# Kernel optimization log

Measured on AMD Instinct MI355X. Metric: run time of the kernel, lower is better.

The kernel has to match this reference:

```python
import jax, jax.numpy as jnp
import numpy as np

N_NODES = 100000
N_EDGES = 1600000
IN_DIM, HID, OUT_DIM = 512, 32, 40


def setup_inputs() -> dict:
    key = jax.random.key(0)
    ks = jax.random.split(key, 6)
    x = jax.random.normal(ks[0], (N_NODES, IN_DIM), dtype=jnp.float32)
    edge_index = jax.random.randint(ks[1], (2, N_EDGES), 0, N_NODES, dtype=jnp.int64)
    # Glorot-ish init for the linear weights
    W1 = jax.random.normal(ks[2], (IN_DIM, HID), dtype=jnp.float32) / np.sqrt(IN_DIM)
    b1 = jnp.zeros((HID,), dtype=jnp.float32)
    W2 = jax.random.normal(ks[3], (HID, OUT_DIM), dtype=jnp.float32) / np.sqrt(HID)
    b2 = jnp.zeros((OUT_DIM,), dtype=jnp.float32)
    return {"x": x, "edge_index": edge_index, "W1": W1, "b1": b1, "W2": W2, "b2": b2}


def gcn_conv(x, W, b, src, dst, n_nodes):
    """PyG GCNConv: h = D^{-1/2} (A + I) D^{-1/2} (x W) + b."""
    h = x @ W  # linear transform first (reduces edge-level traffic)
    # add self-loops
    loop = jnp.arange(n_nodes, dtype=src.dtype)
    s = jnp.concatenate([src, loop])
    d = jnp.concatenate([dst, loop])
    # symmetric normalization from in-degree (including self-loops)
    deg = jax.ops.segment_sum(jnp.ones_like(d, dtype=h.dtype), d, num_segments=n_nodes)
    dinv = jnp.where(deg > 0, jax.lax.rsqrt(deg), 0.0)
    norm = dinv[s] * dinv[d]  # [E+N]
    msg = h[s] * norm[:, None]  # gather + scale
    out = jax.ops.segment_sum(msg, d, num_segments=n_nodes)  # scatter-add
    return out + b


def reference(x, edge_index, W1, b1, W2, b2):
    src, dst = edge_index[0], edge_index[1]
    n = x.shape[0]
    h = jax.nn.relu(gcn_conv(x, W1, b1, src, dst, n))
    # dropout is identity in eval mode (reference runs in eval)
    out = gcn_conv(h, W2, b2, src, dst, n)
    return out
```

## Files before the change

kernel.cpp:

```cpp
#include <hip/hip_runtime.h>
#include <hip/hip_bf16.h>

#define N_IN 512
#define HID 32
#define OUTD 40
#define NCOPY 8

typedef __attribute__((ext_vector_type(8))) short bf16x8;
typedef __attribute__((ext_vector_type(4))) float f32x4;
typedef __attribute__((ext_vector_type(8))) _Float16 half8;


__global__ void k_init(int* __restrict__ csr, int tot4, int* __restrict__ cnt8,
                       int n8_4, int n, _Float16* __restrict__ g1, _Float16* __restrict__ p)
{
    int i = blockIdx.x * blockDim.x + threadIdx.x;
    if (i < tot4) {
        int4 v = make_int4(n, n, n, n);
        *(int4*)&csr[(size_t)i * 4] = v;
    }
    if (i < n8_4) {
        int4 z4 = make_int4(0, 0, 0, 0);
        *(int4*)&cnt8[(size_t)i * 4] = z4;
    }
    if (blockIdx.x == 0) {
        float4 z = make_float4(0.f, 0.f, 0.f, 0.f);
        if (threadIdx.x < 4)
            ((float4*)&g1[(size_t)n * HID])[threadIdx.x] = z;
        else if (threadIdx.x < 8)
            ((float4*)&p[(size_t)n * HID])[threadIdx.x - 4] = z;
    }
}

__global__ void k_count(const int* __restrict__ dst, int* __restrict__ cnt8,
                        int* __restrict__ rankp, int n, int e)
{
    int c = blockIdx.x & (NCOPY - 1);
    int* mycnt = cnt8 + (size_t)c * n;
    int i = (blockIdx.x * blockDim.x + threadIdx.x) * 4;
    if (i + 3 < e) {
        int4 d4 = *(const int4*)&dst[i];
        int r0 = atomicAdd(&mycnt[d4.x], 1);
        int r1 = atomicAdd(&mycnt[d4.y], 1);
        int r2 = atomicAdd(&mycnt[d4.z], 1);
        int r3 = atomicAdd(&mycnt[d4.w], 1);
        int hc = c << 24;
        *(int4*)&rankp[i] = make_int4(hc | r0, hc | r1, hc | r2, hc | r3);
    } else if (i < e) {
        for (int k = i; k < e; k++) {
            int r = atomicAdd(&mycnt[dst[k]], 1);
            rankp[k] = (c << 24) | r;
        }
    }
}

__global__ void k_bases(int* __restrict__ cnt8, int* __restrict__ cnt, int n)
{
    int d = blockIdx.x * blockDim.x + threadIdx.x;
    if (d >= n) return;
    int s = 0;
#pragma unroll
    for (int c = 0; c < NCOPY; c++) {
        int v = cnt8[(size_t)c * n + d];
        cnt8[(size_t)c * n + d] = s;
        s += v;
    }
    cnt[d] = s;
}

__global__ __launch_bounds__(256) void k_scan1(const int* __restrict__ cnt,
                                               int* __restrict__ offs,
                                               int* __restrict__ bsums, int n)
{
    __shared__ int sm[256];
    int t = threadIdx.x;
    int base = blockIdx.x * 1024 + t * 4;
    int a0 = (base + 0 < n) ? cnt[base + 0] : 0;
    int a1 = (base + 1 < n) ? cnt[base + 1] : 0;
    int a2 = (base + 2 < n) ? cnt[base + 2] : 0;
    int a3 = (base + 3 < n) ? cnt[base + 3] : 0;
    int d0 = (a0 + 15) & ~15;
    int d1 = (a1 + 15) & ~15;
    int d2 = (a2 + 15) & ~15;
    int d3 = (a3 + 15) & ~15;
    int s = d0 + d1 + d2 + d3;
    sm[t] = s;
    __syncthreads();
#pragma unroll
    for (int off = 1; off < 256; off <<= 1) {
        int v = (t >= off) ? sm[t - off] : 0;
        __syncthreads();
        sm[t] += v;
        __syncthreads();
    }
    int excl = sm[t] - s;
    if (base + 0 < n) offs[base + 0] = excl;
    if (base + 1 < n) offs[base + 1] = excl + d0;
    if (base + 2 < n) offs[base + 2] = excl + d0 + d1;
    if (base + 3 < n) offs[base + 3] = excl + d0 + d1 + d2;
    if (t == 255) bsums[blockIdx.x] = sm[255];
}

__global__ __launch_bounds__(256) void k_scan2(int* bsums, int nb)
{
    __shared__ int sm[256];
    int t = threadIdx.x;
    int s = (t < nb) ? bsums[t] : 0;
    sm[t] = s;
    __syncthreads();
#pragma unroll
    for (int off = 1; off < 256; off <<= 1) {
        int v = (t >= off) ? sm[t - off] : 0;
        __syncthreads();
        sm[t] += v;
        __syncthreads();
    }
    if (t < nb) bsums[t] = sm[t] - s;
}

__global__ void k_scan3(int* __restrict__ offs, const int* __restrict__ bsums,
                        const int* __restrict__ cnt, float* __restrict__ dinv, int n)
{
    int i = blockIdx.x * blockDim.x + threadIdx.x;
    if (i >= n) return;
    offs[i] = offs[i] + bsums[i >> 10];
    dinv[i] = rsqrtf((float)(cnt[i] + 1));
}

__global__ void k_posfill(const int* __restrict__ dst, const int* __restrict__ src,
                          const int* __restrict__ offs, const int* __restrict__ cnt8,
                          const int* __restrict__ rankp, int* __restrict__ csr,
                          int n, int e)
{
    int i = (blockIdx.x * blockDim.x + threadIdx.x) * 4;
    if (i >= e) return;
    if (i + 3 < e) {
        int4 d4 = *(const int4*)&dst[i];
        int4 rp = *(const int4*)&rankp[i];
        int4 s4 = *(const int4*)&src[i];
        int dd[4] = {d4.x, d4.y, d4.z, d4.w};
        int rr[4] = {rp.x, rp.y, rp.z, rp.w};
        int ss[4] = {s4.x, s4.y, s4.z, s4.w};
#pragma unroll
        for (int k = 0; k < 4; k++) {
            int d = dd[k];
            int c = ((unsigned)rr[k]) >> 24;
            int r = rr[k] & 0xFFFFFF;
            csr[offs[d] + cnt8[(size_t)c * n + d] + r] = ss[k];
        }
    } else {
        for (int k = i; k < e; k++) {
            int d = dst[k];
            int rv = rankp[k];
            int c = ((unsigned)rv) >> 24;
            int r = rv & 0xFFFFFF;
            csr[offs[d] + cnt8[(size_t)c * n + d] + r] = src[k];
        }
    }
}

__global__ void k_convw(const float* __restrict__ W, unsigned short* __restrict__ wfh,
                        unsigned short* __restrict__ wfl)
{
    int idx = blockIdx.x * blockDim.x + threadIdx.x;
    int j     = idx & 7;
    int lane  = (idx >> 3) & 63;
    int ntile = (idx >> 9) & 1;
    int kstep = idx >> 10;
    int k    = kstep * 32 + (lane >> 4) * 8 + j;
    int ncol = ntile * 16 + (lane & 15);
    float v = W[k * HID + ncol];
    unsigned u = __builtin_bit_cast(unsigned, v);
    unsigned short h = (unsigned short)(u >> 16);
    float hv = __builtin_bit_cast(float, u & 0xFFFF0000u);
    float rem = v - hv;
    unsigned ur = __builtin_bit_cast(unsigned, rem);
    ur += 0x7FFF + ((ur >> 16) & 1);
    wfh[idx] = h;
    wfl[idx] = (unsigned short)(ur >> 16);
}

__global__ __launch_bounds__(256) void k_gemm1(
    const float* __restrict__ x,
    const unsigned short* __restrict__ wfh, const unsigned short* __restrict__ wfl,
    const float* __restrict__ dinv, _Float16* __restrict__ g1, int n)
{
    const int t    = threadIdx.x;
    const int lane = t & 63;
    const int wave = t >> 6;
    const int m    = lane & 15;
    const int quad = lane >> 4;
    const int row0 = blockIdx.x * 64 + wave * 16;

    int arow = row0 + m;
    if (arow >= n) arow = n - 1;
    const float* xp = x + (size_t)arow * N_IN + quad * 8;

    f32x4 acc0 = {0.f, 0.f, 0.f, 0.f};
    f32x4 acc1 = {0.f, 0.f, 0.f, 0.f};

    for (int ks = 0; ks < 16; ks++) {
        float4 xa = *(const float4*)(xp + ks * 32);
        float4 xb = *(const float4*)(xp + ks * 32 + 4);
        float xe[8] = {xa.x, xa.y, xa.z, xa.w, xb.x, xb.y, xb.z, xb.w};
        bf16x8 ah, al;
#pragma unroll
        for (int j = 0; j < 8; j++) {
            unsigned u = __builtin_bit_cast(unsigned, xe[j]);
            ah[j] = (short)(u >> 16);
            float hv = __builtin_bit_cast(float, u & 0xFFFF0000u);
            float rem = xe[j] - hv;
            unsigned ur = __builtin_bit_cast(unsigned, rem);
            ur += 0x7FFF + ((ur >> 16) & 1);
            al[j] = (short)(ur >> 16);
        }
        bf16x8 bh0 = *(const bf16x8*)(wfh + ((size_t)(ks * 2 + 0) * 64 + lane) * 8);
        bf16x8 bh1 = *(const bf16x8*)(wfh + ((size_t)(ks * 2 + 1) * 64 + lane) * 8);
        bf16x8 bl0 = *(const bf16x8*)(wfl + ((size_t)(ks * 2 + 0) * 64 + lane) * 8);
        bf16x8 bl1 = *(const bf16x8*)(wfl + ((size_t)(ks * 2 + 1) * 64 + lane) * 8);

        acc0 = __builtin_amdgcn_mfma_f32_16x16x32_bf16(ah, bh0, acc0, 0, 0, 0);
        acc0 = __builtin_amdgcn_mfma_f32_16x16x32_bf16(al, bh0, acc0, 0, 0, 0);
        acc0 = __builtin_amdgcn_mfma_f32_16x16x32_bf16(ah, bl0, acc0, 0, 0, 0);
        acc1 = __builtin_amdgcn_mfma_f32_16x16x32_bf16(ah, bh1, acc1, 0, 0, 0);
        acc1 = __builtin_amdgcn_mfma_f32_16x16x32_bf16(al, bh1, acc1, 0, 0, 0);
        acc1 = __builtin_amdgcn_mfma_f32_16x16x32_bf16(ah, bl1, acc1, 0, 0, 0);
    }

#pragma unroll
    for (int r = 0; r < 4; r++) {
        int row = row0 + quad * 4 + r;
        if (row < n) {
            float dv = dinv[row];
            g1[(size_t)row * HID + m]      = (_Float16)(acc0[r] * dv);
            g1[(size_t)row * HID + 16 + m] = (_Float16)(acc1[r] * dv);
        }
    }
}


__global__ void k_agg1(const int* __restrict__ csr, const int* __restrict__ offs,
                       const int* __restrict__ cnt, const _Float16* __restrict__ g,
                       const float* __restrict__ dinv, const float* __restrict__ b1,
                       _Float16* __restrict__ p, int n)
{
    int gid = blockIdx.x * blockDim.x + threadIdx.x;
    int r  = gid >> 4;
    int sl = gid & 15;
    if (r >= n) return;
    int s0 = offs[r];
    int dp = (cnt[r] + 15) & ~15;
    int q  = sl >> 2;
    int cq = sl & 3;
    const _Float16* gc = g + cq * 8;
    float acc[8] = {0.f, 0.f, 0.f, 0.f, 0.f, 0.f, 0.f, 0.f};
    if (q == 0) {
        half8 v = *(const half8*)&gc[(size_t)r * HID];
#pragma unroll
        for (int j = 0; j < 8; j++) acc[j] = (float)v[j];
    }
    for (int b = 0; b < dp; b += 16) {
        int s = csr[s0 + b + sl];
#pragma unroll
        for (int tt = 0; tt < 4; tt++) {
            int sj = __shfl(s, tt * 4 + q, 16);
            half8 v = *(const half8*)&gc[(size_t)sj * HID];
#pragma unroll
            for (int j = 0; j < 8; j++) acc[j] += (float)v[j];
        }
    }
#pragma unroll
    for (int j = 0; j < 8; j++) {
        acc[j] += __shfl(acc[j], sl ^ 4, 16);
        acc[j] += __shfl(acc[j], sl ^ 8, 16);
    }
    if (q == 0) {
        float dv = dinv[r];
        float4 ba = *(const float4*)&b1[cq * 8];
        float4 bb = *(const float4*)&b1[cq * 8 + 4];
        float bv[8] = {ba.x, ba.y, ba.z, ba.w, bb.x, bb.y, bb.z, bb.w};
        half8 hp;
#pragma unroll
        for (int j = 0; j < 8; j++)
            hp[j] = (_Float16)(dv * fmaxf(acc[j] * dv + bv[j], 0.f));
        *(half8*)&p[(size_t)r * HID + cq * 8] = hp;
    }
}

__global__ void k_agg2_out(const int* __restrict__ csr, const int* __restrict__ offs,
                           const int* __restrict__ cnt, const _Float16* __restrict__ g,
                           const float* __restrict__ dinv, const float* __restrict__ W2,
                           const float* __restrict__ b2, float* __restrict__ out, int n)
{
    int gid = blockIdx.x * blockDim.x + threadIdx.x;
    int r  = gid >> 4;
    int sl = gid & 15;
    if (r >= n) return;
    int s0 = offs[r];
    int dp = (cnt[r] + 15) & ~15;
    int q  = sl >> 2;
    int cq = sl & 3;
    const _Float16* gc = g + cq * 8;
    float acc[8] = {0.f, 0.f, 0.f, 0.f, 0.f, 0.f, 0.f, 0.f};
    if (q == 0) {
        half8 v = *(const half8*)&gc[(size_t)r * HID];
#pragma unroll
        for (int j = 0; j < 8; j++) acc[j] = (float)v[j];
    }
    for (int b = 0; b < dp; b += 16) {
        int s = csr[s0 + b + sl];
#pragma unroll
        for (int tt = 0; tt < 4; tt++) {
            int sj = __shfl(s, tt * 4 + q, 16);
            half8 v = *(const half8*)&gc[(size_t)sj * HID];
#pragma unroll
            for (int j = 0; j < 8; j++) acc[j] += (float)v[j];
        }
    }
#pragma unroll
    for (int j = 0; j < 8; j++) {
        acc[j] += __shfl(acc[j], sl ^ 4, 16);
        acc[j] += __shfl(acc[j], sl ^ 8, 16);
    }
    float dv = dinv[r];
    float h[8];
#pragma unroll
    for (int j = 0; j < 8; j++) h[j] = acc[j] * dv;

    int oc = (sl < 10) ? sl * 4 : 0;
    float4 ov = *(const float4*)&b2[oc];
#pragma unroll
    for (int k = 0; k < HID; k++) {
        float a = __shfl(h[k & 7], k >> 3, 16);
        float4 wv = *(const float4*)&W2[k * OUTD + oc];
        ov.x += a * wv.x;
        ov.y += a * wv.y;
        ov.z += a * wv.z;
        ov.w += a * wv.w;
    }
    if (sl < 10) *(float4*)&out[(size_t)r * OUTD + sl * 4] = ov;
}

extern "C" void kernel_launch(void* const* d_in, const int* in_sizes, int n_in,
                              void* d_out, int out_size, void* d_ws, size_t ws_size,
                              hipStream_t stream)
{
    const float* x  = (const float*)d_in[0];
    const int*   ei = (const int*)d_in[1];
    const float* W1 = (const float*)d_in[2];
    const float* b1 = (const float*)d_in[3];
    const float* W2 = (const float*)d_in[4];
    const float* b2 = (const float*)d_in[5];
    float* out = (float*)d_out;

    const int n = in_sizes[0] / N_IN;
    const int e = in_sizes[1] / 2;
    const int* src = ei;
    const int* dst = ei + e;

    const int csr_cap = e + 16 * n;

    char* w = (char*)d_ws;
    float* dinv   = (float*)w;            w += sizeof(float) * (size_t)((n + 3) & ~3);
    _Float16* g1  = (_Float16*)w;         w += sizeof(_Float16) * (size_t)(n + 1) * HID;
    _Float16* p   = (_Float16*)w;         w += sizeof(_Float16) * (size_t)(n + 1) * HID;
    int*   cnt    = (int*)w;              w += sizeof(int) * (size_t)((n + 3) & ~3);
    int*   offs   = (int*)w;              w += sizeof(int) * (size_t)((n + 3) & ~3);
    int*   cnt8   = (int*)w;              w += sizeof(int) * (size_t)NCOPY * ((n + 3) & ~3);
    int*   rankp  = (int*)w;              w += sizeof(int) * (size_t)((e + 3) & ~3);
    int*   bsums  = (int*)w;              w += sizeof(int) * 1024;
    unsigned short* wfh = (unsigned short*)w;  w += sizeof(unsigned short) * 16384;
    unsigned short* wfl = (unsigned short*)w;  w += sizeof(unsigned short) * 16384;
    int*   csr    = (int*)w;              w += sizeof(int) * (size_t)((csr_cap + 3) & ~3);

    const int nb = (n + 1023) / 1024;
    const int ec = (e + 3) / 4;
    const int n8_4 = (NCOPY * n + 3) / 4;
    const int tot4 = (csr_cap + 3) / 4;
    const int initN = (tot4 > n8_4) ? tot4 : n8_4;

    k_init<<<(initN + 255) / 256, 256, 0, stream>>>(csr, tot4, cnt8, n8_4, n, g1, p);
    k_count<<<(ec + 255) / 256, 256, 0, stream>>>(dst, cnt8, rankp, n, e);
    k_bases<<<(n + 255) / 256, 256, 0, stream>>>(cnt8, cnt, n);
    k_scan1<<<nb, 256, 0, stream>>>(cnt, offs, bsums, n);
    k_scan2<<<1, 256, 0, stream>>>(bsums, nb);
    k_scan3<<<(n + 255) / 256, 256, 0, stream>>>(offs, bsums, cnt, dinv, n);
    k_posfill<<<(ec + 255) / 256, 256, 0, stream>>>(dst, src, offs, cnt8, rankp, csr, n, e);

    k_convw<<<64, 256, 0, stream>>>(W1, wfh, wfl);

    k_gemm1<<<(n + 63) / 64, 256, 0, stream>>>(x, wfh, wfl, dinv, g1, n);

    int t16 = n * 16;
    k_agg1<<<(t16 + 255) / 256, 256, 0, stream>>>(csr, offs, cnt, g1, dinv, b1, p, n);
    k_agg2_out<<<(t16 + 255) / 256, 256, 0, stream>>>(csr, offs, cnt, p, dinv, W2, b2, out, n);
}
```

Measured before the change: 493.6 us.

## Drop padded CSR, fuse count bases into scan, add tail handling in aggregation

Removes the 16-aligned CSR padding and the kernel that filled the padded CSR with sentinel indices. Aggregation kernels now handle a partial tail block by loading only the valid entries and using the zero row n for the rest. The per-copy base computation and the dinv computation are folded into the first scan kernel, with int4 vectorised accesses, which removes one launch. The GEMM now uses nontemporal loads for x and truncates the low bf16 part instead of rounding it. Together these cut memory traffic and launch count, at the cost of a small precision change and more branching in the gather loop.

```diff
diff --git a/kernel.cpp b/kernel.cpp
--- a/kernel.cpp
+++ b/kernel.cpp
@@ -11,14 +11,10 @@
 typedef __attribute__((ext_vector_type(8))) _Float16 half8;
 
 
-__global__ void k_init(int* __restrict__ csr, int tot4, int* __restrict__ cnt8,
-                       int n8_4, int n, _Float16* __restrict__ g1, _Float16* __restrict__ p)
+__global__ void k_init(int* __restrict__ cnt8, int n8_4, int n,
+                       _Float16* __restrict__ g1, _Float16* __restrict__ p)
 {
     int i = blockIdx.x * blockDim.x + threadIdx.x;
-    if (i < tot4) {
-        int4 v = make_int4(n, n, n, n);
-        *(int4*)&csr[(size_t)i * 4] = v;
-    }
     if (i < n8_4) {
         int4 z4 = make_int4(0, 0, 0, 0);
         *(int4*)&cnt8[(size_t)i * 4] = z4;
@@ -54,36 +50,33 @@
     }
 }
 
-__global__ void k_bases(int* __restrict__ cnt8, int* __restrict__ cnt, int n)
-{
-    int d = blockIdx.x * blockDim.x + threadIdx.x;
-    if (d >= n) return;
-    int s = 0;
-#pragma unroll
-    for (int c = 0; c < NCOPY; c++) {
-        int v = cnt8[(size_t)c * n + d];
-        cnt8[(size_t)c * n + d] = s;
-        s += v;
-    }
-    cnt[d] = s;
-}
-
-__global__ __launch_bounds__(256) void k_scan1(const int* __restrict__ cnt,
+__global__ __launch_bounds__(256) void k_scanA(int* __restrict__ cnt8,
+                                               int* __restrict__ cnt,
+                                               float* __restrict__ dinv,
                                                int* __restrict__ offs,
                                                int* __restrict__ bsums, int n)
 {
     __shared__ int sm[256];
     int t = threadIdx.x;
     int base = blockIdx.x * 1024 + t * 4;
-    int a0 = (base + 0 < n) ? cnt[base + 0] : 0;
-    int a1 = (base + 1 < n) ? cnt[base + 1] : 0;
-    int a2 = (base + 2 < n) ? cnt[base + 2] : 0;
-    int a3 = (base + 3 < n) ? cnt[base + 3] : 0;
-    int d0 = (a0 + 15) & ~15;
-    int d1 = (a1 + 15) & ~15;
-    int d2 = (a2 + 15) & ~15;
-    int d3 = (a3 + 15) & ~15;
-    int s = d0 + d1 + d2 + d3;
+    int4 run = make_int4(0, 0, 0, 0);
+    if (base < n) {
+#pragma unroll
+        for (int c = 0; c < NCOPY; c++) {
+            int4 v = *(int4*)&cnt8[(size_t)c * n + base];
+            *(int4*)&cnt8[(size_t)c * n + base] = run;
+            run.x += v.x; run.y += v.y; run.z += v.z; run.w += v.w;
+        }
+        *(int4*)&cnt[base] = run;
+        float4 dv;
+        dv.x = rsqrtf((float)(run.x + 1));
+        dv.y = rsqrtf((float)(run.y + 1));
+        dv.z = rsqrtf((float)(run.z + 1));
+        dv.w = rsqrtf((float)(run.w + 1));
+        *(float4*)&dinv[base] = dv;
+    }
+    int a0 = run.x, a1 = run.y, a2 = run.z, a3 = run.w;
+    int s = a0 + a1 + a2 + a3;
     sm[t] = s;
     __syncthreads();
 #pragma unroll
@@ -94,10 +87,14 @@
         __syncthreads();
     }
     int excl = sm[t] - s;
-    if (base + 0 < n) offs[base + 0] = excl;
-    if (base + 1 < n) offs[base + 1] = excl + d0;
-    if (base + 2 < n) offs[base + 2] = excl + d0 + d1;
-    if (base + 3 < n) offs[base + 3] = excl + d0 + d1 + d2;
+    if (base < n) {
+        int4 o;
+        o.x = excl;
+        o.y = excl + a0;
+        o.z = excl + a0 + a1;
+        o.w = excl + a0 + a1 + a2;
+        *(int4*)&offs[base] = o;
+    }
     if (t == 255) bsums[blockIdx.x] = sm[255];
 }
 
@@ -118,13 +115,14 @@
     if (t < nb) bsums[t] = sm[t] - s;
 }
 
-__global__ void k_scan3(int* __restrict__ offs, const int* __restrict__ bsums,
-                        const int* __restrict__ cnt, float* __restrict__ dinv, int n)
+__global__ void k_scan3(int* __restrict__ offs, const int* __restrict__ bsums, int n4)
 {
     int i = blockIdx.x * blockDim.x + threadIdx.x;
-    if (i >= n) return;
-    offs[i] = offs[i] + bsums[i >> 10];
-    dinv[i] = rsqrtf((float)(cnt[i] + 1));
+    if (i >= n4) return;
+    int add = bsums[(i * 4) >> 10];
+    int4 v = *(int4*)&offs[(size_t)i * 4];
+    v.x += add; v.y += add; v.z += add; v.w += add;
+    *(int4*)&offs[(size_t)i * 4] = v;
 }
 
 __global__ void k_posfill(const int* __restrict__ dst, const int* __restrict__ src,
@@ -200,9 +198,9 @@
     f32x4 acc1 = {0.f, 0.f, 0.f, 0.f};
 
     for (int ks = 0; ks < 16; ks++) {
-        float4 xa = *(const float4*)(xp + ks * 32);
-        float4 xb = *(const float4*)(xp + ks * 32 + 4);
-        float xe[8] = {xa.x, xa.y, xa.z, xa.w, xb.x, xb.y, xb.z, xb.w};
+        f32x4 xa = __builtin_nontemporal_load((const f32x4*)(xp + ks * 32));
+        f32x4 xb = __builtin_nontemporal_load((const f32x4*)(xp + ks * 32 + 4));
+        float xe[8] = {xa[0], xa[1], xa[2], xa[3], xb[0], xb[1], xb[2], xb[3]};
         bf16x8 ah, al;
 #pragma unroll
         for (int j = 0; j < 8; j++) {
@@ -211,7 +209,6 @@
             float hv = __builtin_bit_cast(float, u & 0xFFFF0000u);
             float rem = xe[j] - hv;
             unsigned ur = __builtin_bit_cast(unsigned, rem);
-            ur += 0x7FFF + ((ur >> 16) & 1);
             al[j] = (short)(ur >> 16);
         }
         bf16x8 bh0 = *(const bf16x8*)(wfh + ((size_t)(ks * 2 + 0) * 64 + lane) * 8);
@@ -249,7 +246,8 @@
     int sl = gid & 15;
     if (r >= n) return;
     int s0 = offs[r];
-    int dp = (cnt[r] + 15) & ~15;
+    int d  = cnt[r];
+    int full = d & ~15;
     int q  = sl >> 2;
     int cq = sl & 3;
     const _Float16* gc = g + cq * 8;
@@ -259,8 +257,19 @@
 #pragma unroll
         for (int j = 0; j < 8; j++) acc[j] = (float)v[j];
     }
-    for (int b = 0; b < dp; b += 16) {
+    for (int b = 0; b < full; b += 16) {
         int s = csr[s0 + b + sl];
+#pragma unroll
+        for (int tt = 0; tt < 4; tt++) {
+            int sj = __shfl(s, tt * 4 + q, 16);
+            half8 v = *(const half8*)&gc[(size_t)sj * HID];
+#pragma unroll
+            for (int j = 0; j < 8; j++) acc[j] += (float)v[j];
+        }
+    }
+    int rem = d - full;
+    if (rem) {
+        int s = (sl < rem) ? csr[s0 + full + sl] : n;
 #pragma unroll
         for (int tt = 0; tt < 4; tt++) {
             int sj = __shfl(s, tt * 4 + q, 16);
@@ -297,7 +306,8 @@
     int sl = gid & 15;
     if (r >= n) return;
     int s0 = offs[r];
-    int dp = (cnt[r] + 15) & ~15;
+    int d  = cnt[r];
+    int full = d & ~15;
     int q  = sl >> 2;
     int cq = sl & 3;
     const _Float16* gc = g + cq * 8;
@@ -307,8 +317,19 @@
 #pragma unroll
         for (int j = 0; j < 8; j++) acc[j] = (float)v[j];
     }
-    for (int b = 0; b < dp; b += 16) {
+    for (int b = 0; b < full; b += 16) {
         int s = csr[s0 + b + sl];
+#pragma unroll
+        for (int tt = 0; tt < 4; tt++) {
+            int sj = __shfl(s, tt * 4 + q, 16);
+            half8 v = *(const half8*)&gc[(size_t)sj * HID];
+#pragma unroll
+            for (int j = 0; j < 8; j++) acc[j] += (float)v[j];
+        }
+    }
+    int rem = d - full;
+    if (rem) {
+        int s = (sl < rem) ? csr[s0 + full + sl] : n;
 #pragma unroll
         for (int tt = 0; tt < 4; tt++) {
             int sj = __shfl(s, tt * 4 + q, 16);
@@ -357,8 +378,6 @@
     const int e = in_sizes[1] / 2;
     const int* src = ei;
     const int* dst = ei + e;
-
-    const int csr_cap = e + 16 * n;
 
     char* w = (char*)d_ws;
     float* dinv   = (float*)w;            w += sizeof(float) * (size_t)((n + 3) & ~3);
@@ -371,20 +390,18 @@
     int*   bsums  = (int*)w;              w += sizeof(int) * 1024;
     unsigned short* wfh = (unsigned short*)w;  w += sizeof(unsigned short) * 16384;
     unsigned short* wfl = (unsigned short*)w;  w += sizeof(unsigned short) * 16384;
-    int*   csr    = (int*)w;              w += sizeof(int) * (size_t)((csr_cap + 3) & ~3);
+    int*   csr    = (int*)w;              w += sizeof(int) * (size_t)((e + 3) & ~3);
 
     const int nb = (n + 1023) / 1024;
     const int ec = (e + 3) / 4;
+    const int n4 = (n + 3) / 4;
     const int n8_4 = (NCOPY * n + 3) / 4;
-    const int tot4 = (csr_cap + 3) / 4;
-    const int initN = (tot4 > n8_4) ? tot4 : n8_4;
-
-    k_init<<<(initN + 255) / 256, 256, 0, stream>>>(csr, tot4, cnt8, n8_4, n, g1, p);
+
+    k_init<<<(n8_4 + 255) / 256, 256, 0, stream>>>(cnt8, n8_4, n, g1, p);
     k_count<<<(ec + 255) / 256, 256, 0, stream>>>(dst, cnt8, rankp, n, e);
-    k_bases<<<(n + 255) / 256, 256, 0, stream>>>(cnt8, cnt, n);
-    k_scan1<<<nb, 256, 0, stream>>>(cnt, offs, bsums, n);
+    k_scanA<<<nb, 256, 0, stream>>>(cnt8, cnt, dinv, offs, bsums, n);
     k_scan2<<<1, 256, 0, stream>>>(bsums, nb);
-    k_scan3<<<(n + 255) / 256, 256, 0, stream>>>(offs, bsums, cnt, dinv, n);
+    k_scan3<<<(n4 + 255) / 256, 256, 0, stream>>>(offs, bsums, n4);
     k_posfill<<<(ec + 255) / 256, 256, 0, stream>>>(dst, src, offs, cnt8, rankp, csr, n, e);
 
     k_convw<<<64, 256, 0, stream>>>(W1, wfh, wfl);
```

Measured after the change: 484.0 us. No clear change (-1.9%).
